# Kernel optimization log

Measured on AMD Instinct MI355X. Metric: run time of the kernel, lower is better.

Reference implementation:

```python
import jax, jax.numpy as jnp
import numpy as np

D = 2048; Nl = 2; Nh = 32; Nkv = 8; V = 32000; Dh = 5632; Lm = 4096
B = 1; L = 2048; E = 1e-5
DHEAD = D // Nh  # 64


def setup_inputs() -> dict:
    key = jax.random.key(0)
    ks = jax.random.split(key, 10)
    s = 0.02
    rn = lambda k, shape: jax.random.normal(k, shape, jnp.float32) * s
    emb = rn(ks[0], (V, D))
    wq = rn(ks[1], (Nl, D, D))
    wk = rn(ks[2], (Nl, D, D * Nkv // Nh))
    wv = rn(ks[3], (Nl, D, D * Nkv // Nh))
    wa = rn(ks[4], (Nl, D, D))
    wg = rn(ks[5], (Nl, D, Dh))
    wu = rn(ks[6], (Nl, D, Dh))
    wd = rn(ks[7], (Nl, Dh, D))
    w_an = jnp.ones((Nl, D), jnp.float32)
    w_fn = jnp.ones((Nl, D), jnp.float32)
    w_on = jnp.ones((D,), jnp.float32)
    w_out = rn(ks[8], (D, V))
    # RoPE tables (interleaved-pair convention, matching reshape(..., -1, 2))
    theta = 1.0 / (10000.0 ** (jnp.arange(0, DHEAD, 2, dtype=jnp.float32) / DHEAD))
    freqs = jnp.outer(jnp.arange(Lm, dtype=jnp.float32), theta)  # [Lm, DHEAD//2]
    cos = jnp.cos(freqs)
    sin = jnp.sin(freqs)
    ti = jax.random.randint(ks[9], (B, L), 0, V)
    return dict(ti=ti, emb=emb, wq=wq, wk=wk, wv=wv, wa=wa, w_an=w_an, w_fn=w_fn,
                wg=wg, wu=wu, wd=wd, w_on=w_on, w_out=w_out, cos=cos, sin=sin)


def _rmsnorm(x, w):
    return x * jax.lax.rsqrt(jnp.mean(x * x, -1, keepdims=True) + E) * w


def _rope(x, cos, sin):
    # x: [B, L, H, DHEAD]; cos/sin: [1, L, 1, DHEAD//2]; interleaved pairs
    xs = x.reshape(*x.shape[:-1], DHEAD // 2, 2)
    xr, xi = xs[..., 0], xs[..., 1]
    r1 = xr * cos - xi * sin
    i1 = xr * sin + xi * cos
    return jnp.stack([r1, i1], axis=-1).reshape(x.shape)


def reference(ti, emb, wq, wk, wv, wa, w_an, w_fn, wg, wu, wd, w_on, w_out, cos, sin):
    cos_l = cos[:L].reshape(1, L, 1, DHEAD // 2)
    sin_l = sin[:L].reshape(1, L, 1, DHEAD // 2)
    mask = jnp.triu(jnp.full((1, 1, L, L), -jnp.inf, jnp.float32), 1)
    scale = 1.0 / jnp.sqrt(jnp.float32(DHEAD))
    rep = Nh // Nkv
    x = emb[ti]  # [B, L, D]
    for l in range(Nl):
        h = _rmsnorm(x, w_an[l])
        q = (h @ wq[l]).reshape(B, L, Nh, DHEAD)
        k = (h @ wk[l]).reshape(B, L, Nkv, DHEAD)
        v = (h @ wv[l]).reshape(B, L, Nkv, DHEAD)
        q = _rope(q, cos_l, sin_l)
        k = _rope(k, cos_l, sin_l)
        kx = jnp.repeat(k, rep, axis=2)  # GQA expand -> [B, L, Nh, DHEAD]
        vx = jnp.repeat(v, rep, axis=2)
        a = jnp.einsum('blhd,bmhd->bhlm', q, kx) * scale
        p = jax.nn.softmax(a + mask, axis=-1)
        sa = jnp.einsum('bhlm,bmhd->blhd', p, vx).reshape(B, L, D)
        x = x + sa @ wa[l]
        hf = _rmsnorm(x, w_fn[l])
        x = x + (jax.nn.silu(hf @ wg[l]) * (hf @ wu[l])) @ wd[l]
    return _rmsnorm(x, w_on) @ w_out  # [B, L, V]
```

## Files before the change

### kernel.cpp

```cpp
#include <hip/hip_runtime.h>
#include <hip/hip_bf16.h>

#define DMODEL 2048
#define LSEQ   2048
#define NHEAD  32
#define NKVH   8
#define DHEAD  64
#define DFF    5632
#define VOCAB  32000

typedef __attribute__((ext_vector_type(8))) short bf16x8;
typedef __attribute__((ext_vector_type(4))) float f32x4;
typedef __attribute__((ext_vector_type(8))) unsigned short ushort8;

__device__ __forceinline__ void gload_lds16(const __hip_bfloat16* g, __hip_bfloat16* l) {
  __builtin_amdgcn_global_load_lds((const void __attribute__((address_space(1)))*)g,
                                   (void __attribute__((address_space(3)))*)l, 16, 0, 0);
}

__device__ __forceinline__ float bfbits2f(unsigned short u) {
  return __uint_as_float(((unsigned int)u) << 16);
}
__device__ __forceinline__ unsigned short f2bfbits(float f) {
  unsigned int x = __float_as_uint(f);
  return (unsigned short)((x + 0x7fffu + ((x >> 16) & 1u)) >> 16);
}

__global__ __launch_bounds__(256) void embed_k(const int* __restrict__ ti,
                                               const float* __restrict__ emb,
                                               float* __restrict__ x) {
  const int row = blockIdx.x;
  const int t = threadIdx.x;
  const int tok = ti[row];
  const float4* s = (const float4*)(emb + (size_t)tok * DMODEL);
  float4* d = (float4*)(x + (size_t)row * DMODEL);
  d[t] = s[t];
  d[t + 256] = s[t + 256];
}

__global__ __launch_bounds__(256) void rmsnorm_k(const float* __restrict__ x,
                                                 const float* __restrict__ w,
                                                 __hip_bfloat16* __restrict__ out) {
  const int row = blockIdx.x;
  const int t = threadIdx.x;
  const float4* xr = (const float4*)(x + (size_t)row * DMODEL);
  float4 a = xr[t];
  float4 b = xr[t + 256];
  float ss = a.x*a.x + a.y*a.y + a.z*a.z + a.w*a.w
           + b.x*b.x + b.y*b.y + b.z*b.z + b.w*b.w;
  #pragma unroll
  for (int m = 32; m >= 1; m >>= 1) ss += __shfl_xor(ss, m);
  __shared__ float red[4];
  if ((t & 63) == 0) red[t >> 6] = ss;
  __syncthreads();
  const float tot = red[0] + red[1] + red[2] + red[3];
  const float sc = rsqrtf(tot * (1.0f / DMODEL) + 1e-5f);
  const float4* w4 = (const float4*)w;
  float4 wa_ = w4[t], wb_ = w4[t + 256];
  __hip_bfloat16* o = out + (size_t)row * DMODEL;
  o[4*t + 0] = __float2bfloat16(a.x * sc * wa_.x);
  o[4*t + 1] = __float2bfloat16(a.y * sc * wa_.y);
  o[4*t + 2] = __float2bfloat16(a.z * sc * wa_.z);
  o[4*t + 3] = __float2bfloat16(a.w * sc * wa_.w);
  o[1024 + 4*t + 0] = __float2bfloat16(b.x * sc * wb_.x);
  o[1024 + 4*t + 1] = __float2bfloat16(b.y * sc * wb_.y);
  o[1024 + 4*t + 2] = __float2bfloat16(b.z * sc * wb_.z);
  o[1024 + 4*t + 3] = __float2bfloat16(b.w * sc * wb_.w);
}

__global__ __launch_bounds__(256) void transpose_k(const float* __restrict__ src,
                                                   __hip_bfloat16* __restrict__ dst,
                                                   int K, int N) {
  __shared__ float tile[64 * 65];
  const int kb = blockIdx.x * 64;
  const int nb = blockIdx.y * 64;
  const int t = threadIdx.x;
  #pragma unroll
  for (int i = 0; i < 16; ++i) {
    const int idx = t + 256 * i;
    const int r = idx >> 6, c = idx & 63;
    tile[r * 65 + c] = src[(size_t)(kb + r) * N + nb + c];
  }
  __syncthreads();
  #pragma unroll
  for (int i = 0; i < 16; ++i) {
    const int idx = t + 256 * i;
    const int n = idx >> 6, k = idx & 63;
    dst[(size_t)(nb + n) * K + kb + k] = __float2bfloat16(tile[k * 65 + n]);
  }
}

template <int EPI>
__global__ __launch_bounds__(256) void gemm_bt(const __hip_bfloat16* __restrict__ A,
                                               const __hip_bfloat16* __restrict__ Bt,
                                               float* __restrict__ Cf,
                                               __hip_bfloat16* __restrict__ Cb,
                                               int M, int N, int K) {
  __shared__ __align__(16) __hip_bfloat16 As[128 * 32];
  __shared__ __align__(16) __hip_bfloat16 Bs[128 * 32];
  const int tid = threadIdx.x;
  const int wave = tid >> 6;
  const int lane = tid & 63;
  const int nbx = M >> 7;
  const int nwg = nbx * (N >> 7);
  const int orig = blockIdx.y * nbx + blockIdx.x;
  const int wid = (orig & 7) * (nwg >> 3) + (orig >> 3);
  const int tm = (wid % nbx) << 7;
  const int tn = (wid / nbx) << 7;
  const int wr = (wave >> 1) * 64;
  const int wc = (wave & 1) * 64;
  const int fr = lane & 15;
  const int fg = lane >> 4;
  const f32x4 fzero = {0.f, 0.f, 0.f, 0.f};
  f32x4 acc[4][4];
  #pragma unroll
  for (int i = 0; i < 4; ++i)
    #pragma unroll
    for (int j = 0; j < 4; ++j) acc[i][j] = fzero;
  const int srow = wave * 32 + (lane >> 2);
  const int scol = (lane & 3) * 8;
  const __hip_bfloat16* gA = A + (size_t)(tm + srow) * K + scol;
  const __hip_bfloat16* gB = Bt + (size_t)(tn + srow) * K + scol;
  __hip_bfloat16* lA = &As[wave * 1024];
  __hip_bfloat16* lB = &Bs[wave * 1024];
  for (int k0 = 0; k0 < K; k0 += 32) {
    gload_lds16(gA, lA);
    gload_lds16(gA + (size_t)16 * K, lA + 512);
    gload_lds16(gB, lB);
    gload_lds16(gB + (size_t)16 * K, lB + 512);
    gA += 32; gB += 32;
    __syncthreads();
    bf16x8 af[4], bfr[4];
    #pragma unroll
    for (int i = 0; i < 4; ++i) af[i] = *(const bf16x8*)&As[(wr + i * 16 + fr) * 32 + fg * 8];
    #pragma unroll
    for (int j = 0; j < 4; ++j) bfr[j] = *(const bf16x8*)&Bs[(wc + j * 16 + fr) * 32 + fg * 8];
    #pragma unroll
    for (int i = 0; i < 4; ++i)
      #pragma unroll
      for (int j = 0; j < 4; ++j)
        acc[i][j] = __builtin_amdgcn_mfma_f32_16x16x32_bf16(af[i], bfr[j], acc[i][j], 0, 0, 0);
    __syncthreads();
  }
  #pragma unroll
  for (int i = 0; i < 4; ++i)
    #pragma unroll
    for (int j = 0; j < 4; ++j)
      #pragma unroll
      for (int r = 0; r < 4; ++r) {
        const int row = tm + wr + i * 16 + fg * 4 + r;
        const int col = tn + wc + j * 16 + fr;
        const float v = acc[i][j][r];
        if (EPI == 0) Cf[(size_t)row * N + col] = v;
        else if (EPI == 1) Cb[(size_t)row * N + col] = __float2bfloat16(v);
        else Cf[(size_t)row * N + col] += v;
      }
}

template <int EPI>
__global__ __launch_bounds__(512, 2) void gemm8p(const __hip_bfloat16* __restrict__ A,
                                                 const __hip_bfloat16* __restrict__ Bt,
                                                 float* __restrict__ Cf,
                                                 __hip_bfloat16* __restrict__ Cb,
                                                 int M, int N, int K) {
  __shared__ __align__(16) __hip_bfloat16 lds[2][2][256 * 64];
  const int tid = threadIdx.x;
  const int wave = tid >> 6;
  const int lane = tid & 63;
  const int nbx = M >> 8;
  const int nwg = nbx * (N >> 8);
  const int orig = blockIdx.y * nbx + blockIdx.x;
  const int wid = (orig & 7) * (nwg >> 3) + (orig >> 3);
  const int tm = (wid % nbx) << 8;
  const int tn = (wid / nbx) << 8;
  const int wm = wave >> 2;
  const int wn = wave & 3;
  const int fr = lane & 15;
  const int fg = lane >> 4;
  const int l3 = lane >> 3;
  const int l7 = lane & 7;
  const int swzcol = (l3 ^ l7) << 3;
  const size_t sK = (size_t)K;

  const __hip_bfloat16* pA = A + (size_t)(tm + wave * 8 + l3) * sK + swzcol;
  const __hip_bfloat16* pB = Bt + (size_t)(tn + wave * 8 + l3) * sK + swzcol;

  #pragma unroll
  for (int j = 0; j < 4; ++j) {
    gload_lds16(pA + (size_t)(j * 64) * sK, &lds[0][0][(j * 64 + wave * 8) * 64]);
    gload_lds16(pB + (size_t)(j * 64) * sK, &lds[0][1][(j * 64 + wave * 8) * 64]);
  }
  pA += 64; pB += 64;
  #pragma unroll
  for (int j = 0; j < 4; ++j) {
    gload_lds16(pA + (size_t)(j * 64) * sK, &lds[1][0][(j * 64 + wave * 8) * 64]);
    gload_lds16(pB + (size_t)(j * 64) * sK, &lds[1][1][(j * 64 + wave * 8) * 64]);
  }
  pA += 64; pB += 64;

  const f32x4 fzero = {0.f, 0.f, 0.f, 0.f};
  f32x4 acc[8][4];
  #pragma unroll
  for (int i = 0; i < 8; ++i)
    #pragma unroll
    for (int j = 0; j < 4; ++j) acc[i][j] = fzero;

  const int wmo = wm * 128;
  const int wno = wn * 64;
  const int rswz = (fr & 7) << 4;
  const int ct0 = ((fg * 16) ^ rswz) >> 1;
  const int ct1 = ((64 + fg * 16) ^ rswz) >> 1;

  asm volatile("s_waitcnt vmcnt(8)" ::: "memory");
  __builtin_amdgcn_s_barrier();
  __builtin_amdgcn_sched_barrier(0);

  const int NT = K >> 6;
  for (int kt = 0; kt < NT; ++kt) {
    const int cur = kt & 1;
    const __hip_bfloat16* LA = &lds[cur][0][0];
    const __hip_bfloat16* LB = &lds[cur][1][0];
    bf16x8 av[8][2], bv[4][2];
    #pragma unroll
    for (int mi = 0; mi < 8; ++mi) {
      av[mi][0] = *(const bf16x8*)&LA[(wmo + mi * 16 + fr) * 64 + ct0];
      av[mi][1] = *(const bf16x8*)&LA[(wmo + mi * 16 + fr) * 64 + ct1];
    }
    #pragma unroll
    for (int ni = 0; ni < 4; ++ni) {
      bv[ni][0] = *(const bf16x8*)&LB[(wno + ni * 16 + fr) * 64 + ct0];
      bv[ni][1] = *(const bf16x8*)&LB[(wno + ni * 16 + fr) * 64 + ct1];
    }
    asm volatile("s_waitcnt lgkmcnt(0)" ::: "memory");
    __builtin_amdgcn_sched_barrier(0);
    __builtin_amdgcn_s_barrier();
    __builtin_amdgcn_sched_barrier(0);
    const bool pre = (kt + 2 < NT);
    #pragma unroll
    for (int q = 0; q < 4; ++q) {
      if (pre) {
        gload_lds16(pA + (size_t)(q * 64) * sK, &lds[cur][0][(q * 64 + wave * 8) * 64]);
        gload_lds16(pB + (size_t)(q * 64) * sK, &lds[cur][1][(q * 64 + wave * 8) * 64]);
      }
      const int mb = (q & 1) * 4;
      const int nb = (q >> 1) * 2;
      __builtin_amdgcn_s_setprio(1);
      #pragma unroll
      for (int mi = 0; mi < 4; ++mi)
        #pragma unroll
        for (int ni = 0; ni < 2; ++ni) {
          acc[mb + mi][nb + ni] = __builtin_amdgcn_mfma_f32_16x16x32_bf16(
              av[mb + mi][0], bv[nb + ni][0], acc[mb + mi][nb + ni], 0, 0, 0);
          acc[mb + mi][nb + ni] = __builtin_amdgcn_mfma_f32_16x16x32_bf16(
              av[mb + mi][1], bv[nb + ni][1], acc[mb + mi][nb + ni], 0, 0, 0);
        }
      __builtin_amdgcn_s_setprio(0);
    }
    if (pre) { pA += 64; pB += 64; }
    if (kt + 1 < NT) {
      if (pre) asm volatile("s_waitcnt vmcnt(8)" ::: "memory");
      else     asm volatile("s_waitcnt vmcnt(0)" ::: "memory");
      __builtin_amdgcn_s_barrier();
      __builtin_amdgcn_sched_barrier(0);
    }
  }
  #pragma unroll
  for (int mf = 0; mf < 8; ++mf)
    #pragma unroll
    for (int nf = 0; nf < 4; ++nf)
      #pragma unroll
      for (int r = 0; r < 4; ++r) {
        const int row = tm + wmo + mf * 16 + fg * 4 + r;
        const int col = tn + wno + nf * 16 + fr;
        const float v = acc[mf][nf][r];
        if (EPI == 0) Cf[(size_t)row * N + col] = v;
        else if (EPI == 1) Cb[(size_t)row * N + col] = __float2bfloat16(v);
        else Cf[(size_t)row * N + col] += v;
      }
}

__global__ __launch_bounds__(256) void rope_k(__hip_bfloat16* __restrict__ qkv,
                                              const float* __restrict__ cosT,
                                              const float* __restrict__ sinT) {
  const int row = blockIdx.x;
  const int t = threadIdx.x;
  unsigned int* base = (unsigned int*)(qkv + (size_t)row * 3072);
  #pragma unroll
  for (int p = t; p < 1280; p += 256) {
    const int hp = p >> 5;
    const int i = p & 31;
    const unsigned int packed = base[hp * 32 + i];
    const float x0 = bfbits2f((unsigned short)(packed & 0xffffu));
    const float x1 = bfbits2f((unsigned short)(packed >> 16));
    const float c = cosT[row * 32 + i];
    const float s = sinT[row * 32 + i];
    const float r0 = x0 * c - x1 * s;
    const float r1 = x0 * s + x1 * c;
    base[hp * 32 + i] = (unsigned int)f2bfbits(r0) | ((unsigned int)f2bfbits(r1) << 16);
  }
}

__global__ __launch_bounds__(256) void attn_k(const __hip_bfloat16* __restrict__ qkv,
                                              __hip_bfloat16* __restrict__ out) {
  const int h = blockIdx.x;
  const int qt = blockIdx.y;
  const int tid = threadIdx.x;
  const int wave = tid >> 6;
  const int lane = tid & 63;
  const int fr = lane & 15;
  const int fg = lane >> 4;
  const int qb = qt * 64;
  const int kcol = DMODEL + (h >> 2) * DHEAD;
  const int vcol = DMODEL + NKVH * DHEAD + (h >> 2) * DHEAD;
  __shared__ __align__(16) __hip_bfloat16 Ks[64 * 72];
  __shared__ __align__(16) __hip_bfloat16 Vt[64 * 72];
  __shared__ __align__(16) __hip_bfloat16 Ps[4][16 * 72];
  bf16x8 qf[2];
  {
    const __hip_bfloat16* qp = qkv + (size_t)(qb + wave * 16 + fr) * 3072 + h * DHEAD + fg * 8;
    qf[0] = *(const bf16x8*)qp;
    qf[1] = *(const bf16x8*)(qp + 32);
  }
  const f32x4 fzero = {0.f, 0.f, 0.f, 0.f};
  float m_run = -1e30f, l_run = 0.f;
  f32x4 o[4];
  #pragma unroll
  for (int c = 0; c < 4; ++c) o[c] = fzero;

  const int sr = tid >> 2;
  const int sc = (tid & 3) * 16;
  const int vpr = tid >> 3;
  const int vg = tid & 7;
  const int myq = qb + wave * 16 + fr;

  for (int t = 0; t <= qt; ++t) {
    const __hip_bfloat16* kp = qkv + (size_t)(t * 64 + sr) * 3072 + kcol + sc;
    *(float4*)&Ks[sr * 72 + sc] = *(const float4*)kp;
    *(float4*)&Ks[sr * 72 + sc + 8] = *(const float4*)(kp + 8);
    {
      const __hip_bfloat16* vp0 = qkv + (size_t)(t * 64 + 2 * vpr) * 3072 + vcol + vg * 8;
      ushort8 va = *(const ushort8*)vp0;
      ushort8 vb = *(const ushort8*)(vp0 + 3072);
      unsigned short* vt = (unsigned short*)Vt;
      #pragma unroll
      for (int i = 0; i < 8; ++i) {
        unsigned int pk = (unsigned int)va[i] | ((unsigned int)vb[i] << 16);
        *(unsigned int*)(vt + (vg * 8 + i) * 72 + 2 * vpr) = pk;
      }
    }
    __syncthreads();
    f32x4 s[4];
    #pragma unroll
    for (int c = 0; c < 4; ++c) {
      s[c] = fzero;
      #pragma unroll
      for (int ks = 0; ks < 2; ++ks) {
        bf16x8 kf = *(const bf16x8*)&Ks[(c * 16 + fr) * 72 + ks * 32 + fg * 8];
        s[c] = __builtin_amdgcn_mfma_f32_16x16x32_bf16(kf, qf[ks], s[c], 0, 0, 0);
      }
    }
    float pm = -1e30f;
    #pragma unroll
    for (int c = 0; c < 4; ++c)
      #pragma unroll
      for (int r = 0; r < 4; ++r) {
        float v = s[c][r] * 0.125f;
        if (t * 64 + c * 16 + fg * 4 + r > myq) v = -1e30f;
        s[c][r] = v;
        pm = fmaxf(pm, v);
      }
    pm = fmaxf(pm, __shfl_xor(pm, 16));
    pm = fmaxf(pm, __shfl_xor(pm, 32));
    const float mn = fmaxf(m_run, pm);
    const float al = __expf(m_run - mn);
    m_run = mn;
    float rs = 0.f;
    #pragma unroll
    for (int c = 0; c < 4; ++c)
      #pragma unroll
      for (int r = 0; r < 4; ++r) {
        float p = __expf(s[c][r] - mn);
        s[c][r] = p;
        rs += p;
      }
    rs += __shfl_xor(rs, 16);
    rs += __shfl_xor(rs, 32);
    l_run = l_run * al + rs;
    float als[4];
    #pragma unroll
    for (int r = 0; r < 4; ++r) als[r] = __shfl(al, fg * 4 + r);
    #pragma unroll
    for (int c = 0; c < 4; ++c)
      #pragma unroll
      for (int r = 0; r < 4; ++r) o[c][r] *= als[r];
    {
      unsigned short* pw = (unsigned short*)Ps[wave];
      #pragma unroll
      for (int c = 0; c < 4; ++c) {
        unsigned int lo = (unsigned int)f2bfbits(s[c][0]) | ((unsigned int)f2bfbits(s[c][1]) << 16);
        unsigned int hi = (unsigned int)f2bfbits(s[c][2]) | ((unsigned int)f2bfbits(s[c][3]) << 16);
        uint2 pk; pk.x = lo; pk.y = hi;
        *(uint2*)(pw + fr * 72 + c * 16 + fg * 4) = pk;
      }
    }
    #pragma unroll
    for (int ks = 0; ks < 2; ++ks) {
      bf16x8 pf = *(const bf16x8*)&Ps[wave][fr * 72 + ks * 32 + fg * 8];
      #pragma unroll
      for (int c = 0; c < 4; ++c) {
        bf16x8 vf = *(const bf16x8*)&Vt[(c * 16 + fr) * 72 + ks * 32 + fg * 8];
        o[c] = __builtin_amdgcn_mfma_f32_16x16x32_bf16(pf, vf, o[c], 0, 0, 0);
      }
    }
    __syncthreads();
  }
  float lq[4];
  #pragma unroll
  for (int r = 0; r < 4; ++r) lq[r] = __shfl(l_run, fg * 4 + r);
  #pragma unroll
  for (int c = 0; c < 4; ++c)
    #pragma unroll
    for (int r = 0; r < 4; ++r)
      out[(size_t)(qb + wave * 16 + fg * 4 + r) * DMODEL + h * DHEAD + c * 16 + fr] =
          __float2bfloat16(o[c][r] / lq[r]);
}

__global__ __launch_bounds__(256) void silu_k(const __hip_bfloat16* __restrict__ gu,
                                              __hip_bfloat16* __restrict__ mb) {
  const int row = blockIdx.x;
  const int t = threadIdx.x;
  const ushort8* g8 = (const ushort8*)(gu + (size_t)row * (2 * DFF));
  const ushort8* u8 = (const ushort8*)(gu + (size_t)row * (2 * DFF) + DFF);
  ushort8* m8 = (ushort8*)(mb + (size_t)row * DFF);
  for (int j = t; j * 8 < DFF; j += 256) {
    ushort8 g = g8[j], u = u8[j];
    ushort8 ov;
    #pragma unroll
    for (int i = 0; i < 8; ++i) {
      const float gf = bfbits2f(g[i]);
      const float uf = bfbits2f(u[i]);
      ov[i] = f2bfbits(gf / (1.f + __expf(-gf)) * uf);
    }
    m8[j] = ov;
  }
}

extern "C" void kernel_launch(void* const* d_in, const int* in_sizes, int n_in,
                              void* d_out, int out_size, void* d_ws, size_t ws_size,
                              hipStream_t stream) {
  const int* ti = (const int*)d_in[0];
  const float* emb = (const float*)d_in[1];
  const float* wq = (const float*)d_in[2];
  const float* wk = (const float*)d_in[3];
  const float* wv = (const float*)d_in[4];
  const float* wa = (const float*)d_in[5];
  const float* w_an = (const float*)d_in[6];
  const float* w_fn = (const float*)d_in[7];
  const float* wg = (const float*)d_in[8];
  const float* wu = (const float*)d_in[9];
  const float* wd = (const float*)d_in[10];
  const float* w_on = (const float*)d_in[11];
  const float* w_out = (const float*)d_in[12];
  const float* cosT = (const float*)d_in[13];
  const float* sinT = (const float*)d_in[14];
  float* outp = (float*)d_out;

  char* ws = (char*)d_ws;
  float* x            = (float*)(ws + 0);
  __hip_bfloat16* h   = (__hip_bfloat16*)(ws + 16777216);
  __hip_bfloat16* qkv = (__hip_bfloat16*)(ws + 25165824);
  __hip_bfloat16* att = (__hip_bfloat16*)(ws + 37748736);
  __hip_bfloat16* gu  = (__hip_bfloat16*)(ws + 46137344);
  __hip_bfloat16* mb  = (__hip_bfloat16*)(ws + 92274688);
  __hip_bfloat16* wTqkv = (__hip_bfloat16*)(ws + 115343360);
  __hip_bfloat16* wTa   = (__hip_bfloat16*)(ws + 127926272);
  __hip_bfloat16* wTgu  = (__hip_bfloat16*)(ws + 136314880);
  __hip_bfloat16* wTd   = (__hip_bfloat16*)(ws + 182452224);
  __hip_bfloat16* wTout = (__hip_bfloat16*)(ws + 25165824);
  (void)in_sizes; (void)n_in; (void)out_size; (void)ws_size;

  const dim3 blk(256);
  embed_k<<<2048, blk, 0, stream>>>(ti, emb, x);
  for (int l = 0; l < 2; ++l) {
    transpose_k<<<dim3(32, 32), blk, 0, stream>>>(wq + (size_t)l * 2048 * 2048, wTqkv, 2048, 2048);
    transpose_k<<<dim3(32, 8),  blk, 0, stream>>>(wk + (size_t)l * 2048 * 512, wTqkv + (size_t)2048 * 2048, 2048, 512);
    transpose_k<<<dim3(32, 8),  blk, 0, stream>>>(wv + (size_t)l * 2048 * 512, wTqkv + (size_t)2560 * 2048, 2048, 512);
    transpose_k<<<dim3(32, 32), blk, 0, stream>>>(wa + (size_t)l * 2048 * 2048, wTa, 2048, 2048);
    transpose_k<<<dim3(32, 88), blk, 0, stream>>>(wg + (size_t)l * 2048 * 5632, wTgu, 2048, 5632);
    transpose_k<<<dim3(32, 88), blk, 0, stream>>>(wu + (size_t)l * 2048 * 5632, wTgu + (size_t)5632 * 2048, 2048, 5632);
    transpose_k<<<dim3(88, 32), blk, 0, stream>>>(wd + (size_t)l * 5632 * 2048, wTd, 5632, 2048);

    rmsnorm_k<<<2048, blk, 0, stream>>>(x, w_an + l * 2048, h);
    gemm_bt<1><<<dim3(16, 24), blk, 0, stream>>>(h, wTqkv, nullptr, qkv, 2048, 3072, 2048);
    rope_k<<<2048, blk, 0, stream>>>(qkv, cosT, sinT);
    attn_k<<<dim3(32, 32), blk, 0, stream>>>(qkv, att);
    gemm_bt<2><<<dim3(16, 16), blk, 0, stream>>>(att, wTa, x, nullptr, 2048, 2048, 2048);

    rmsnorm_k<<<2048, blk, 0, stream>>>(x, w_fn + l * 2048, h);
    gemm8p<1><<<dim3(8, 44), dim3(512), 0, stream>>>(h, wTgu, nullptr, gu, 2048, 11264, 2048);
    silu_k<<<2048, blk, 0, stream>>>(gu, mb);
    gemm_bt<2><<<dim3(16, 16), blk, 0, stream>>>(mb, wTd, x, nullptr, 2048, 2048, 5632);
  }
  transpose_k<<<dim3(32, 500), blk, 0, stream>>>(w_out, wTout, 2048, 32000);
  rmsnorm_k<<<2048, blk, 0, stream>>>(x, w_on, h);
  gemm8p<0><<<dim3(8, 125), dim3(512), 0, stream>>>(h, wTout, outp, nullptr, 2048, 32000, 2048);
}
```

Baseline: 1.427 ms.

## Fuse SiLU gating into gate/up GEMM epilogue; swizzled direct-to-LDS K loads

The gate and up weight transposes now write interleaved rows, so adjacent output columns of the fused GEMM hold a matching gate/up pair. The GEMM epilogue pairs them with a lane shuffle, applies SiLU(g)*u, and writes the half-width activation directly. This removes the separate silu kernel and the round trip of the large intermediate gate/up tensor through memory. Separately, attention loads K tiles with global_load_lds into an XOR-swizzled unpadded LDS layout instead of staging them through registers.

```diff
diff --git a/kernel.cpp b/kernel.cpp
--- a/kernel.cpp
+++ b/kernel.cpp
@@ -70,7 +70,7 @@
 
 __global__ __launch_bounds__(256) void transpose_k(const float* __restrict__ src,
                                                    __hip_bfloat16* __restrict__ dst,
-                                                   int K, int N) {
+                                                   int K, int N, int rstride, int roff) {
   __shared__ float tile[64 * 65];
   const int kb = blockIdx.x * 64;
   const int nb = blockIdx.y * 64;
@@ -86,7 +86,7 @@
   for (int i = 0; i < 16; ++i) {
     const int idx = t + 256 * i;
     const int n = idx >> 6, k = idx & 63;
-    dst[(size_t)(nb + n) * K + kb + k] = __float2bfloat16(tile[k * 65 + n]);
+    dst[((size_t)(nb + n) * rstride + roff) * K + kb + k] = __float2bfloat16(tile[k * 65 + n]);
   }
 }
 
@@ -275,7 +275,14 @@
         const float v = acc[mf][nf][r];
         if (EPI == 0) Cf[(size_t)row * N + col] = v;
         else if (EPI == 1) Cb[(size_t)row * N + col] = __float2bfloat16(v);
-        else Cf[(size_t)row * N + col] += v;
+        else if (EPI == 3) {
+          const float p = __shfl_xor(v, 1);
+          if (!(fr & 1)) {
+            const float sv = v / (1.f + __expf(-v)) * p;
+            Cb[(size_t)row * (N >> 1) + ((tn + wno + nf * 16) >> 1) + (fr >> 1)] =
+                __float2bfloat16(sv);
+          }
+        }
       }
 }
 
@@ -312,7 +319,7 @@
   const int qb = qt * 64;
   const int kcol = DMODEL + (h >> 2) * DHEAD;
   const int vcol = DMODEL + NKVH * DHEAD + (h >> 2) * DHEAD;
-  __shared__ __align__(16) __hip_bfloat16 Ks[64 * 72];
+  __shared__ __align__(16) __hip_bfloat16 Ks[64 * 64];
   __shared__ __align__(16) __hip_bfloat16 Vt[64 * 72];
   __shared__ __align__(16) __hip_bfloat16 Ps[4][16 * 72];
   bf16x8 qf[2];
@@ -327,16 +334,19 @@
   #pragma unroll
   for (int c = 0; c < 4; ++c) o[c] = fzero;
 
-  const int sr = tid >> 2;
-  const int sc = (tid & 3) * 16;
+  const int kr8 = lane >> 3;
+  const int kgr = ((lane & 7) ^ kr8) << 3;
   const int vpr = tid >> 3;
   const int vg = tid & 7;
   const int myq = qb + wave * 16 + fr;
+  const int fr7 = fr & 7;
 
   for (int t = 0; t <= qt; ++t) {
-    const __hip_bfloat16* kp = qkv + (size_t)(t * 64 + sr) * 3072 + kcol + sc;
-    *(float4*)&Ks[sr * 72 + sc] = *(const float4*)kp;
-    *(float4*)&Ks[sr * 72 + sc + 8] = *(const float4*)(kp + 8);
+    {
+      const __hip_bfloat16* kp = qkv + (size_t)(t * 64 + wave * 16 + kr8) * 3072 + kcol + kgr;
+      gload_lds16(kp, &Ks[(wave * 16) * 64]);
+      gload_lds16(kp + (size_t)8 * 3072, &Ks[(wave * 16 + 8) * 64]);
+    }
     {
       const __hip_bfloat16* vp0 = qkv + (size_t)(t * 64 + 2 * vpr) * 3072 + vcol + vg * 8;
       ushort8 va = *(const ushort8*)vp0;
@@ -355,7 +365,7 @@
       s[c] = fzero;
       #pragma unroll
       for (int ks = 0; ks < 2; ++ks) {
-        bf16x8 kf = *(const bf16x8*)&Ks[(c * 16 + fr) * 72 + ks * 32 + fg * 8];
+        bf16x8 kf = *(const bf16x8*)&Ks[(c * 16 + fr) * 64 + (((ks * 4 + fg) ^ fr7) << 3)];
         s[c] = __builtin_amdgcn_mfma_f32_16x16x32_bf16(kf, qf[ks], s[c], 0, 0, 0);
       }
     }
@@ -423,26 +433,6 @@
     for (int r = 0; r < 4; ++r)
       out[(size_t)(qb + wave * 16 + fg * 4 + r) * DMODEL + h * DHEAD + c * 16 + fr] =
           __float2bfloat16(o[c][r] / lq[r]);
-}
-
-__global__ __launch_bounds__(256) void silu_k(const __hip_bfloat16* __restrict__ gu,
-                                              __hip_bfloat16* __restrict__ mb) {
-  const int row = blockIdx.x;
-  const int t = threadIdx.x;
-  const ushort8* g8 = (const ushort8*)(gu + (size_t)row * (2 * DFF));
-  const ushort8* u8 = (const ushort8*)(gu + (size_t)row * (2 * DFF) + DFF);
-  ushort8* m8 = (ushort8*)(mb + (size_t)row * DFF);
-  for (int j = t; j * 8 < DFF; j += 256) {
-    ushort8 g = g8[j], u = u8[j];
-    ushort8 ov;
-    #pragma unroll
-    for (int i = 0; i < 8; ++i) {
-      const float gf = bfbits2f(g[i]);
-      const float uf = bfbits2f(u[i]);
-      ov[i] = f2bfbits(gf / (1.f + __expf(-gf)) * uf);
-    }
-    m8[j] = ov;
-  }
 }
 
 extern "C" void kernel_launch(void* const* d_in, const int* in_sizes, int n_in,
@@ -470,7 +460,6 @@
   __hip_bfloat16* h   = (__hip_bfloat16*)(ws + 16777216);
   __hip_bfloat16* qkv = (__hip_bfloat16*)(ws + 25165824);
   __hip_bfloat16* att = (__hip_bfloat16*)(ws + 37748736);
-  __hip_bfloat16* gu  = (__hip_bfloat16*)(ws + 46137344);
   __hip_bfloat16* mb  = (__hip_bfloat16*)(ws + 92274688);
   __hip_bfloat16* wTqkv = (__hip_bfloat16*)(ws + 115343360);
   __hip_bfloat16* wTa   = (__hip_bfloat16*)(ws + 127926272);
@@ -482,13 +471,13 @@
   const dim3 blk(256);
   embed_k<<<2048, blk, 0, stream>>>(ti, emb, x);
   for (int l = 0; l < 2; ++l) {
-    transpose_k<<<dim3(32, 32), blk, 0, stream>>>(wq + (size_t)l * 2048 * 2048, wTqkv, 2048, 2048);
-    transpose_k<<<dim3(32, 8),  blk, 0, stream>>>(wk + (size_t)l * 2048 * 512, wTqkv + (size_t)2048 * 2048, 2048, 512);
-    transpose_k<<<dim3(32, 8),  blk, 0, stream>>>(wv + (size_t)l * 2048 * 512, wTqkv + (size_t)2560 * 2048, 2048, 512);
-    transpose_k<<<dim3(32, 32), blk, 0, stream>>>(wa + (size_t)l * 2048 * 2048, wTa, 2048, 2048);
-    transpose_k<<<dim3(32, 88), blk, 0, stream>>>(wg + (size_t)l * 2048 * 5632, wTgu, 2048, 5632);
-    transpose_k<<<dim3(32, 88), blk, 0, stream>>>(wu + (size_t)l * 2048 * 5632, wTgu + (size_t)5632 * 2048, 2048, 5632);
-    transpose_k<<<dim3(88, 32), blk, 0, stream>>>(wd + (size_t)l * 5632 * 2048, wTd, 5632, 2048);
+    transpose_k<<<dim3(32, 32), blk, 0, stream>>>(wq + (size_t)l * 2048 * 2048, wTqkv, 2048, 2048, 1, 0);
+    transpose_k<<<dim3(32, 8),  blk, 0, stream>>>(wk + (size_t)l * 2048 * 512, wTqkv + (size_t)2048 * 2048, 2048, 512, 1, 0);
+    transpose_k<<<dim3(32, 8),  blk, 0, stream>>>(wv + (size_t)l * 2048 * 512, wTqkv + (size_t)2560 * 2048, 2048, 512, 1, 0);
+    transpose_k<<<dim3(32, 32), blk, 0, stream>>>(wa + (size_t)l * 2048 * 2048, wTa, 2048, 2048, 1, 0);
+    transpose_k<<<dim3(32, 88), blk, 0, stream>>>(wg + (size_t)l * 2048 * 5632, wTgu, 2048, 5632, 2, 0);
+    transpose_k<<<dim3(32, 88), blk, 0, stream>>>(wu + (size_t)l * 2048 * 5632, wTgu, 2048, 5632, 2, 1);
+    transpose_k<<<dim3(88, 32), blk, 0, stream>>>(wd + (size_t)l * 5632 * 2048, wTd, 5632, 2048, 1, 0);
 
     rmsnorm_k<<<2048, blk, 0, stream>>>(x, w_an + l * 2048, h);
     gemm_bt<1><<<dim3(16, 24), blk, 0, stream>>>(h, wTqkv, nullptr, qkv, 2048, 3072, 2048);
@@ -497,11 +486,10 @@
     gemm_bt<2><<<dim3(16, 16), blk, 0, stream>>>(att, wTa, x, nullptr, 2048, 2048, 2048);
 
     rmsnorm_k<<<2048, blk, 0, stream>>>(x, w_fn + l * 2048, h);
-    gemm8p<1><<<dim3(8, 44), dim3(512), 0, stream>>>(h, wTgu, nullptr, gu, 2048, 11264, 2048);
-    silu_k<<<2048, blk, 0, stream>>>(gu, mb);
+    gemm8p<3><<<dim3(8, 44), dim3(512), 0, stream>>>(h, wTgu, nullptr, mb, 2048, 11264, 2048);
     gemm_bt<2><<<dim3(16, 16), blk, 0, stream>>>(mb, wTd, x, nullptr, 2048, 2048, 5632);
   }
-  transpose_k<<<dim3(32, 500), blk, 0, stream>>>(w_out, wTout, 2048, 32000);
+  transpose_k<<<dim3(32, 500), blk, 0, stream>>>(w_out, wTout, 2048, 32000, 1, 0);
   rmsnorm_k<<<2048, blk, 0, stream>>>(x, w_on, h);
   gemm8p<0><<<dim3(8, 125), dim3(512), 0, stream>>>(h, wTout, outp, nullptr, 2048, 32000, 2048);
 }
```

Measured after the change: 1.424 ms. Within noise of the previous version (-0.2%).
